# Kernel tuning notes

Measured on AMD Instinct MI355X. Metric: run time of the kernel, lower is better.

The kernel has to match this reference:

```python
import jax, jax.numpy as jnp
import numpy as np

B, S, F = 256, 192, 64
HD, L, PRED = 1024, 2, 48


def setup_inputs() -> dict:
    key = jax.random.key(0)
    ks = jax.random.split(key, 9)
    s_in = 1.0 / np.sqrt(F)
    s_h = 1.0 / np.sqrt(HD)
    return {
        "x": jax.random.normal(ks[0], (B, S, F), dtype=jnp.float32),
        "W_hidden": jax.random.uniform(ks[1], (F, HD), jnp.float32, -s_in, s_in),
        "b_hidden": jax.random.uniform(ks[2], (HD,), jnp.float32, -s_in, s_in),
        "Wih": jax.random.uniform(ks[3], (L, HD, HD), jnp.float32, -s_h, s_h),
        "Whh": jax.random.uniform(ks[4], (L, HD, HD), jnp.float32, -s_h, s_h),
        "bih": jax.random.uniform(ks[5], (L, HD), jnp.float32, -s_h, s_h),
        "bhh": jax.random.uniform(ks[6], (L, HD), jnp.float32, -s_h, s_h),
        "Wo": jax.random.uniform(ks[7], (HD, F), jnp.float32, -s_h, s_h),
        "bo": jax.random.uniform(ks[8], (F,), jnp.float32, -s_h, s_h),
    }


def reference(x, W_hidden, b_hidden, Wih, Whh, bih, bhh, Wo, bo):
    # x: [B, S, F]
    x_concat = x @ W_hidden + b_hidden          # [B, S, HD]
    xs = jnp.swapaxes(x_concat, 0, 1)           # [S, B, HD] for time scan
    h0 = jnp.zeros((L, x.shape[0], HD), x.dtype)

    def step(h, x_t):
        # h: [L, B, HD], x_t: [B, HD]; standard tanh-RNN stacked layers
        inp = x_t
        new_h = []
        for l in range(L):
            hl = jnp.tanh(inp @ Wih[l] + bih[l] + h[l] @ Whh[l] + bhh[l])
            new_h.append(hl)
            inp = hl
        h_new = jnp.stack(new_h)
        return h_new, h_new[-1]

    _, ys = jax.lax.scan(step, h0, xs)           # ys: [S, B, HD] top-layer states
    # torch code stores h for t in [0, S-2] only (drops last timestep)
    H = jnp.swapaxes(ys[:-1], 0, 1)              # [B, S-1, HD]
    H = jax.nn.relu(H)
    out = H @ Wo + bo                            # [B, S-1, F]
    return out[:, -PRED:, :]
```

## Files before the change

### kernel.cpp

```cpp
#include <hip/hip_runtime.h>
#include <hip/hip_bf16.h>

#define B    256
#define S    192
#define F    64
#define HD   1024
#define PRED 48
#define TSTART (S - 1 - PRED)
#define NSLOT 48

typedef __attribute__((ext_vector_type(8))) short short8;
typedef __attribute__((ext_vector_type(4))) float f32x4;
typedef unsigned int u32;

static __device__ __forceinline__ short f2bf(float f) {
    __hip_bfloat16 h = __float2bfloat16(f);
    return *reinterpret_cast<short*>(&h);
}
static __device__ __forceinline__ f32x4 mfma16(short8 a, short8 b, f32x4 c) {
    return __builtin_amdgcn_mfma_f32_16x16x32_bf16(a, b, c, 0, 0, 0);
}
static __device__ __forceinline__ short8 ld8(const short* p) {
    return *reinterpret_cast<const short8*>(p);
}
static __device__ __forceinline__ void st_state(short* p, short v) {
    __hip_atomic_store(p, v, __ATOMIC_RELAXED, __HIP_MEMORY_SCOPE_AGENT);
}
static __device__ __forceinline__ u32 ld_flag(const u32* p) {
    return __hip_atomic_load(p, __ATOMIC_RELAXED, __HIP_MEMORY_SCOPE_AGENT);
}
static __device__ __forceinline__ void st_flag(u32* p, u32 v) {
    __hip_atomic_store(p, v, __ATOMIC_RELAXED, __HIP_MEMORY_SCOPE_AGENT);
}

__global__ void fold_kernel(const float* __restrict__ Wh,
                            const float* __restrict__ Wih0,
                            float* __restrict__ Wfold) {
    const int n = (blockIdx.x & 3) * 256 + threadIdx.x;
    const int f = blockIdx.x >> 2;
    float a = 0.f;
#pragma unroll 16
    for (int k = 0; k < HD; ++k)
        a += Wh[f * HD + k] * Wih0[(size_t)k * HD + n];
    Wfold[f * HD + n] = a;
}

__global__ void bias_kernel(const float* __restrict__ bh,
                            const float* __restrict__ Wih0,
                            const float* __restrict__ bih,
                            const float* __restrict__ bhh,
                            float* __restrict__ bf0,
                            float* __restrict__ bf1) {
    __shared__ float red[256];
    const int nl = threadIdx.x & 15;
    const int kc = threadIdx.x >> 4;
    const int n  = blockIdx.x * 16 + nl;
    float a = 0.f;
#pragma unroll 8
    for (int k = kc * 64; k < kc * 64 + 64; ++k)
        a += bh[k] * Wih0[(size_t)k * HD + n];
    red[threadIdx.x] = a;
    __syncthreads();
    if (kc == 0) {
        float s = 0.f;
#pragma unroll
        for (int j = 0; j < 16; ++j) s += red[j * 16 + nl];
        bf0[n] = s + bih[n] + bhh[n];
        bf1[n] = bih[HD + n] + bhh[HD + n];
    }
}

__global__ void transpose_cast(const float* __restrict__ src,
                               short* __restrict__ dst, int K, int N) {
    __shared__ float tile[64][65];
    const int nk = K >> 6;
    const int bk = blockIdx.x % nk;
    const int bn = blockIdx.x / nk;
    const int i  = threadIdx.x;
    {
        const int c4 = (i & 15) * 4;
        for (int it = 0; it < 4; ++it) {
            const int k = (i >> 4) + it * 16;
            const float4 v = *reinterpret_cast<const float4*>(
                &src[(size_t)(bk * 64 + k) * N + bn * 64 + c4]);
            tile[k][c4 + 0] = v.x; tile[k][c4 + 1] = v.y;
            tile[k][c4 + 2] = v.z; tile[k][c4 + 3] = v.w;
        }
    }
    __syncthreads();
    {
        const int n  = i >> 2;
        const int kb = (i & 3) * 16;
        short* dp = &dst[(size_t)(bn * 64 + n) * K + bk * 64 + kb];
#pragma unroll
        for (int j = 0; j < 16; ++j) dp[j] = f2bf(tile[kb + j][n]);
    }
}

__global__ void xcast(const float* __restrict__ x, short* __restrict__ xb) {
    const size_t i = ((size_t)blockIdx.x * 256 + threadIdx.x) * 4;
    const float4 v = *reinterpret_cast<const float4*>(&x[i]);
    short4 o;
    o.x = f2bf(v.x); o.y = f2bf(v.y); o.z = f2bf(v.z); o.w = f2bf(v.w);
    *reinterpret_cast<short4*>(&xb[i]) = o;
}

static __device__ __forceinline__ void stageA(char* lds, const short* __restrict__ src,
                                              int row0) {
    const int tid = threadIdx.x;
#pragma unroll
    for (int it = 0; it < 8; ++it) {
        const int idx = it * 512 + tid;
        const int r   = (idx >> 2) & 31;
        const int off = ((idx >> 7) << 6) + ((idx & 3) << 4);
        const f32x4 v = *reinterpret_cast<const f32x4*>(
            (const char*)src + (size_t)(row0 + r) * 2048 + off);
        *reinterpret_cast<f32x4*>(lds + (idx << 4)) = v;
    }
}

static __device__ __forceinline__ f32x4 gemmLG(const char* ldsA,
                                               const short* __restrict__ bp) {
    f32x4 acc0 = {0.f,0.f,0.f,0.f}, acc1 = {0.f,0.f,0.f,0.f};
    short8 b0[8], b1[8];
#pragma unroll
    for (int j = 0; j < 8; ++j) b0[j] = ld8(bp + j * 32);
#pragma unroll
    for (int c = 0; c < 4; ++c) {
        if (c < 3) {
            short8* nxt = (c & 1) ? b0 : b1;
#pragma unroll
            for (int j = 0; j < 8; ++j) nxt[j] = ld8(bp + (c + 1) * 256 + j * 32);
        }
        const short8* cur = (c & 1) ? b1 : b0;
#pragma unroll
        for (int j = 0; j < 8; ++j) {
            const short8 a = *reinterpret_cast<const short8*>(
                ldsA + (c * 8 + j) * 2048);
            if (j & 1) acc1 = mfma16(a, cur[j], acc1);
            else       acc0 = mfma16(a, cur[j], acc0);
        }
    }
    return acc0 + acc1;
}

__global__ __launch_bounds__(512, 1) void rnn_pers(
    const short* __restrict__ xbf,
    const short* __restrict__ WfoldT, const float* __restrict__ bf0,
    const short* __restrict__ WhhT0, const short* __restrict__ WihT1,
    const short* __restrict__ WhhT1, const float* __restrict__ bf1,
    short* h0h, short* h1h, u32* flags0, u32* flags1) {

    extern __shared__ char lds[];

    const int bid   = blockIdx.x;
    const int layer = bid >> 7;
    const int lb    = bid & 127;
    const int rt    = lb >> 4;
    const int ct    = lb & 15;
    const int w     = threadIdx.x >> 6;
    const int mh    = w & 1;
    const int nq    = w >> 1;
    const int l     = threadIdx.x & 63;
    const int lr    = l & 15, kg = l >> 4;
    const int row0  = rt * 32;
    const int m0    = row0 + mh * 16;
    const int n0    = ct * 64 + nq * 16;
    const int col   = n0 + lr;
    const int rb    = m0 + kg * 4;
    const char* ldsA = lds + mh * 1024 + lr * 64 + kg * 16;

    const float bb = (layer ? bf1 : bf0)[col];
    u32* myflag = (layer ? flags1 : flags0) + (rt * 16 + ct) * 32;
    const int tid = threadIdx.x;

    if (layer == 0) {
        for (int k = 0; k < S - 1; ++k) {
            if (k > 0) {
                __syncthreads();
                if (tid < 16) {
                    const u32* f = flags0 + (rt * 16 + tid) * 32;
                    while (ld_flag(f) < (u32)k) __builtin_amdgcn_s_sleep(1);
                } else if (tid < 32 && k >= 46) {
                    const u32* f = flags1 + (rt * 16 + (tid - 16)) * 32;
                    while (ld_flag(f) < (u32)(k - 45)) __builtin_amdgcn_s_sleep(1);
                }
                __syncthreads();
                stageA(lds, h0h + (size_t)((k - 1) % NSLOT) * B * HD, row0);
                __syncthreads();
            }
            f32x4 acc = {0.f, 0.f, 0.f, 0.f};
            const short* xp = xbf + ((size_t)(m0 + lr) * S + k) * F + kg * 8;
            const short* wf = WfoldT + (size_t)col * F + kg * 8;
            acc = mfma16(ld8(xp),      ld8(wf),      acc);
            acc = mfma16(ld8(xp + 32), ld8(wf + 32), acc);
            if (k > 0)
                acc += gemmLG(ldsA, WhhT0 + (size_t)col * HD + kg * 8);
            short* hd = h0h + (size_t)(k % NSLOT) * B * HD;
#pragma unroll
            for (int r = 0; r < 4; ++r)
                st_state(&hd[(size_t)(rb + r) * HD + col],
                         f2bf(tanhf(acc[r] + bb)));
            __syncthreads();
            if (tid == 0) st_flag(myflag, (u32)(k + 1));
        }
    } else {
        if (tid == 0) st_flag(myflag, 1u);
        for (int k = 1; k < S; ++k) {
            const int t = k - 1;
            __syncthreads();
            if (tid < 16) {
                const u32* f = flags0 + (rt * 16 + tid) * 32;
                while (ld_flag(f) < (u32)k) __builtin_amdgcn_s_sleep(1);
            } else if (tid < 32) {
                const u32* f = flags1 + (rt * 16 + (tid - 16)) * 32;
                while (ld_flag(f) < (u32)k) __builtin_amdgcn_s_sleep(1);
            }
            __syncthreads();
            stageA(lds, h0h + (size_t)((k - 1) % NSLOT) * B * HD, row0);
            f32x4 pre[8];
            if (t > 0) {
                const char* hsrc = (const char*)(h1h
                    + (size_t)((t - 1) % NSLOT) * B * HD);
#pragma unroll
                for (int it = 0; it < 8; ++it) {
                    const int idx = it * 512 + tid;
                    const int r   = (idx >> 2) & 31;
                    const int off = ((idx >> 7) << 6) + ((idx & 3) << 4);
                    pre[it] = *reinterpret_cast<const f32x4*>(
                        hsrc + (size_t)(row0 + r) * 2048 + off);
                }
            }
            __syncthreads();
            f32x4 acc = gemmLG(ldsA, WihT1 + (size_t)col * HD + kg * 8);
            if (t > 0) {
                __syncthreads();
#pragma unroll
                for (int it = 0; it < 8; ++it) {
                    const int idx = it * 512 + tid;
                    *reinterpret_cast<f32x4*>(lds + (idx << 4)) = pre[it];
                }
                __syncthreads();
                acc += gemmLG(ldsA, WhhT1 + (size_t)col * HD + kg * 8);
            }
#pragma unroll
            for (int r = 0; r < 4; ++r)
                st_state(&h1h[(size_t)(t % NSLOT) * B * HD
                              + (size_t)(rb + r) * HD + col],
                         f2bf(tanhf(acc[r] + bb)));
            __syncthreads();
            if (tid == 0) st_flag(myflag, (u32)(k + 1));
        }
    }
}

__global__ __launch_bounds__(256) void outgemm(
    const short* __restrict__ h1h, const short* __restrict__ WoT,
    const float* __restrict__ bo, float* __restrict__ out) {
    const int w = threadIdx.x >> 6, l = threadIdx.x & 63;
    const int lr = l & 15, kg = l >> 4;
    const int m0 = blockIdx.x * 64 + w * 16;
    const int arow = m0 + lr;
    const u32 bidx = (u32)arow / 48u;
    const u32 p    = (u32)arow % 48u;
    const u32 slot = (143u + p) % 48u;

    f32x4 acc[4] = {{0.f,0.f,0.f,0.f},{0.f,0.f,0.f,0.f},
                    {0.f,0.f,0.f,0.f},{0.f,0.f,0.f,0.f}};
    const short* ap = h1h + ((size_t)slot * B + bidx) * HD + kg * 8;
    const short* bp = WoT + (size_t)lr * HD + kg * 8;
#pragma unroll 4
    for (int k0 = 0; k0 < HD; k0 += 32) {
        short8 a = ld8(ap + k0);
#pragma unroll
        for (int j = 0; j < 8; ++j) a[j] = (a[j] < 0) ? (short)0 : a[j];
#pragma unroll
        for (int c = 0; c < 4; ++c)
            acc[c] = mfma16(a, ld8(bp + (size_t)c * 16 * HD + k0), acc[c]);
    }
    const int rb = m0 + kg * 4;
#pragma unroll
    for (int c = 0; c < 4; ++c) {
        const float bbv = bo[c * 16 + lr];
#pragma unroll
        for (int r = 0; r < 4; ++r)
            out[(size_t)(rb + r) * F + c * 16 + lr] = acc[c][r] + bbv;
    }
}

extern "C" void kernel_launch(void* const* d_in, const int* in_sizes, int n_in,
                              void* d_out, int out_size, void* d_ws, size_t ws_size,
                              hipStream_t stream) {
    const float* x   = (const float*)d_in[0];
    const float* Wh  = (const float*)d_in[1];
    const float* bh  = (const float*)d_in[2];
    const float* Wih = (const float*)d_in[3];
    const float* Whh = (const float*)d_in[4];
    const float* bih = (const float*)d_in[5];
    const float* bhh = (const float*)d_in[6];
    const float* Wo  = (const float*)d_in[7];
    const float* bo  = (const float*)d_in[8];
    float* out = (float*)d_out;

    char* p = (char*)d_ws;
    float* Wfold  = (float*)p; p += (size_t)F * HD * 4;
    float* bf0    = (float*)p; p += HD * 4;
    float* bf1    = (float*)p; p += HD * 4;
    short* WfoldT = (short*)p; p += (size_t)HD * F * 2;
    short* WhhT0  = (short*)p; p += (size_t)HD * HD * 2;
    short* WihT1  = (short*)p; p += (size_t)HD * HD * 2;
    short* WhhT1  = (short*)p; p += (size_t)HD * HD * 2;
    short* WoT    = (short*)p; p += (size_t)F * HD * 2;
    short* h0h    = (short*)p; p += (size_t)NSLOT * B * HD * 2;
    short* h1h    = (short*)p; p += (size_t)NSLOT * B * HD * 2;
    short* xbf    = (short*)p; p += (size_t)B * S * F * 2;
    u32*   sync   = (u32*)p;  p += 65536;

    hipMemsetAsync(sync, 0, 65536, stream);

    fold_kernel<<<256, 256, 0, stream>>>(Wh, Wih, Wfold);
    bias_kernel<<<64, 256, 0, stream>>>(bh, Wih, bih, bhh, bf0, bf1);
    transpose_cast<<<16, 256, 0, stream>>>(Wfold, WfoldT, F, HD);
    transpose_cast<<<256, 256, 0, stream>>>(Whh, WhhT0, HD, HD);
    transpose_cast<<<256, 256, 0, stream>>>(Wih + (size_t)HD * HD, WihT1, HD, HD);
    transpose_cast<<<256, 256, 0, stream>>>(Whh + (size_t)HD * HD, WhhT1, HD, HD);
    transpose_cast<<<16, 256, 0, stream>>>(Wo, WoT, HD, F);
    xcast<<<(B * S * F) / (256 * 4), 256, 0, stream>>>(x, xbf);

    u32* flags0 = sync;
    u32* flags1 = sync + 4096;
    void* args[] = {
        (void*)&xbf, (void*)&WfoldT, (void*)&bf0, (void*)&WhhT0,
        (void*)&WihT1, (void*)&WhhT1, (void*)&bf1,
        (void*)&h0h, (void*)&h1h, (void*)&flags0, (void*)&flags1
    };
    hipLaunchCooperativeKernel((void*)rnn_pers, dim3(256), dim3(512),
                               args, 65536, stream);

    outgemm<<<192, 256, 0, stream>>>(h1h, WoT, bo, out);
}
```

Measured before the change: 2.194 ms.

## Double LDS staging for layer-1 RNN and hoist x/Wfold loads out of sync path

Layer 1 now stages both the layer-0 and the previous layer-1 hidden state into LDS at once, using 128KB of dynamic LDS, so the two GEMMs run back to back without the extra barriers and register round trip between them. Staging loads become nontemporal. Layer 0 hoists the Wfold fragments out of the time loop and issues the x loads before the flag spin-wait. gemmLG takes an accumulator input, removing a separate vector add. The larger LDS footprint relies on 160KB LDS per CU and could limit residency if other resources change.

```diff
diff --git a/kernel.cpp b/kernel.cpp
--- a/kernel.cpp
+++ b/kernel.cpp
@@ -105,7 +105,7 @@
     *reinterpret_cast<short4*>(&xb[i]) = o;
 }
 
-static __device__ __forceinline__ void stageA(char* lds, const short* __restrict__ src,
+static __device__ __forceinline__ void stage1(char* lds, const short* __restrict__ src,
                                               int row0) {
     const int tid = threadIdx.x;
 #pragma unroll
@@ -113,15 +113,37 @@
         const int idx = it * 512 + tid;
         const int r   = (idx >> 2) & 31;
         const int off = ((idx >> 7) << 6) + ((idx & 3) << 4);
-        const f32x4 v = *reinterpret_cast<const f32x4*>(
-            (const char*)src + (size_t)(row0 + r) * 2048 + off);
+        const f32x4 v = __builtin_nontemporal_load(
+            reinterpret_cast<const f32x4*>(
+                (const char*)src + (size_t)(row0 + r) * 2048 + off));
         *reinterpret_cast<f32x4*>(lds + (idx << 4)) = v;
     }
 }
 
+static __device__ __forceinline__ void stage2(char* lds,
+                                              const short* __restrict__ s0,
+                                              const short* __restrict__ s1,
+                                              int row0) {
+    const int tid = threadIdx.x;
+#pragma unroll
+    for (int it = 0; it < 8; ++it) {
+        const int idx = it * 512 + tid;
+        const int r   = (idx >> 2) & 31;
+        const int off = ((idx >> 7) << 6) + ((idx & 3) << 4);
+        const size_t g = (size_t)(row0 + r) * 2048 + off;
+        const f32x4 a = __builtin_nontemporal_load(
+            reinterpret_cast<const f32x4*>((const char*)s0 + g));
+        const f32x4 b = __builtin_nontemporal_load(
+            reinterpret_cast<const f32x4*>((const char*)s1 + g));
+        *reinterpret_cast<f32x4*>(lds + (idx << 4)) = a;
+        *reinterpret_cast<f32x4*>(lds + 65536 + (idx << 4)) = b;
+    }
+}
+
 static __device__ __forceinline__ f32x4 gemmLG(const char* ldsA,
-                                               const short* __restrict__ bp) {
-    f32x4 acc0 = {0.f,0.f,0.f,0.f}, acc1 = {0.f,0.f,0.f,0.f};
+                                               const short* __restrict__ bp,
+                                               f32x4 acc_in) {
+    f32x4 acc0 = acc_in, acc1 = {0.f,0.f,0.f,0.f};
     short8 b0[8], b1[8];
 #pragma unroll
     for (int j = 0; j < 8; ++j) b0[j] = ld8(bp + j * 32);
@@ -175,7 +197,12 @@
     const int tid = threadIdx.x;
 
     if (layer == 0) {
+        const short* wf = WfoldT + (size_t)col * F + kg * 8;
+        const short8 wf0 = ld8(wf), wf1 = ld8(wf + 32);
         for (int k = 0; k < S - 1; ++k) {
+            const short* xp = xbf + ((size_t)(m0 + lr) * S + k) * F + kg * 8;
+            const short8 xa0 = ld8(xp);
+            const short8 xa1 = ld8(xp + 32);
             if (k > 0) {
                 __syncthreads();
                 if (tid < 16) {
@@ -186,16 +213,14 @@
                     while (ld_flag(f) < (u32)(k - 45)) __builtin_amdgcn_s_sleep(1);
                 }
                 __syncthreads();
-                stageA(lds, h0h + (size_t)((k - 1) % NSLOT) * B * HD, row0);
+                stage1(lds, h0h + (size_t)((k - 1) % NSLOT) * B * HD, row0);
                 __syncthreads();
             }
             f32x4 acc = {0.f, 0.f, 0.f, 0.f};
-            const short* xp = xbf + ((size_t)(m0 + lr) * S + k) * F + kg * 8;
-            const short* wf = WfoldT + (size_t)col * F + kg * 8;
-            acc = mfma16(ld8(xp),      ld8(wf),      acc);
-            acc = mfma16(ld8(xp + 32), ld8(wf + 32), acc);
+            acc = mfma16(xa0, wf0, acc);
+            acc = mfma16(xa1, wf1, acc);
             if (k > 0)
-                acc += gemmLG(ldsA, WhhT0 + (size_t)col * HD + kg * 8);
+                acc = gemmLG(ldsA, WhhT0 + (size_t)col * HD + kg * 8, acc);
             short* hd = h0h + (size_t)(k % NSLOT) * B * HD;
 #pragma unroll
             for (int r = 0; r < 4; ++r)
@@ -217,32 +242,18 @@
                 while (ld_flag(f) < (u32)k) __builtin_amdgcn_s_sleep(1);
             }
             __syncthreads();
-            stageA(lds, h0h + (size_t)((k - 1) % NSLOT) * B * HD, row0);
-            f32x4 pre[8];
+            const short* h0src = h0h + (size_t)((k - 1) % NSLOT) * B * HD;
             if (t > 0) {
-                const char* hsrc = (const char*)(h1h
-                    + (size_t)((t - 1) % NSLOT) * B * HD);
-#pragma unroll
-                for (int it = 0; it < 8; ++it) {
-                    const int idx = it * 512 + tid;
-                    const int r   = (idx >> 2) & 31;
-                    const int off = ((idx >> 7) << 6) + ((idx & 3) << 4);
-                    pre[it] = *reinterpret_cast<const f32x4*>(
-                        hsrc + (size_t)(row0 + r) * 2048 + off);
-                }
+                stage2(lds, h0src,
+                       h1h + (size_t)((t - 1) % NSLOT) * B * HD, row0);
+            } else {
+                stage1(lds, h0src, row0);
             }
             __syncthreads();
-            f32x4 acc = gemmLG(ldsA, WihT1 + (size_t)col * HD + kg * 8);
-            if (t > 0) {
-                __syncthreads();
-#pragma unroll
-                for (int it = 0; it < 8; ++it) {
-                    const int idx = it * 512 + tid;
-                    *reinterpret_cast<f32x4*>(lds + (idx << 4)) = pre[it];
-                }
-                __syncthreads();
-                acc += gemmLG(ldsA, WhhT1 + (size_t)col * HD + kg * 8);
-            }
+            f32x4 acc = {0.f, 0.f, 0.f, 0.f};
+            acc = gemmLG(ldsA, WihT1 + (size_t)col * HD + kg * 8, acc);
+            if (t > 0)
+                acc = gemmLG(ldsA + 65536, WhhT1 + (size_t)col * HD + kg * 8, acc);
 #pragma unroll
             for (int r = 0; r < 4; ++r)
                 st_state(&h1h[(size_t)(t % NSLOT) * B * HD
@@ -335,7 +346,7 @@
         (void*)&h0h, (void*)&h1h, (void*)&flags0, (void*)&flags1
     };
     hipLaunchCooperativeKernel((void*)rnn_pers, dim3(256), dim3(512),
-                               args, 65536, stream);
+                               args, 131072, stream);
 
     outgemm<<<192, 256, 0, stream>>>(h1h, WoT, bo, out);
 }
```

Measured after the change: 3.075 ms. 1.4x slower.
